# Kernel optimization log

Hardware: AMD Instinct MI355X
Metric: run time of the kernel (lower is better)

## Reference

```python
import jax, jax.numpy as jnp
import numpy as np

POI, EMB, UNITS, QDIM, B = 5000, 256, 512, 256, 64


def setup_inputs() -> dict:
    key = jax.random.key(0)
    ks = jax.random.split(key, 16)
    s = 0.05
    return {
        "x": jax.random.randint(ks[0], (B,), 0, POI),
        "query": jax.random.normal(ks[1], (B, QDIM), jnp.float32),
        "poi_embedding": jax.random.normal(ks[2], (POI, EMB), jnp.float32),
        "A_hat": jax.random.normal(ks[3], (B, B), jnp.float32),
        "dec_hidden": jax.random.normal(ks[4], (B, UNITS), jnp.float32),
        "cat_dec_hidden": jax.random.normal(ks[5], (1, B, UNITS), jnp.float32),
        # GRUCell params (keras order z, r, h; reset_after=True -> bias [2, 3*units])
        "gru_kernel": jax.random.normal(ks[6], (EMB + QDIM, 3 * UNITS), jnp.float32) * s,
        "gru_rec_kernel": jax.random.normal(ks[7], (UNITS, 3 * UNITS), jnp.float32) * s,
        "gru_bias": jax.random.normal(ks[8], (2, 3 * UNITS), jnp.float32) * s,
        # Bahdanau attention params
        "W1_w": jax.random.normal(ks[9], (EMB, UNITS), jnp.float32) * s,
        "W1_b": jnp.zeros((UNITS,), jnp.float32),
        "W2_w": jax.random.normal(ks[10], (UNITS, UNITS), jnp.float32) * s,
        "W2_b": jnp.zeros((UNITS,), jnp.float32),
        "V_w": jax.random.normal(ks[11], (UNITS, 1), jnp.float32) * s,
        "V_b": jnp.zeros((1,), jnp.float32),
        # output dense: concat(context EMB, output_ UNITS, cat_hidden UNITS) -> POI
        "fc_w": jax.random.normal(ks[12], (EMB + 2 * UNITS, POI), jnp.float32) * s,
        "fc_b": jnp.zeros((POI,), jnp.float32),
    }


def _gru_cell(x, h, kernel, rec_kernel, bias):
    # keras GRUCell, reset_after=True, gate order (z, r, h)
    xm = x @ kernel + bias[0]        # [B, 3U]
    hm = h @ rec_kernel + bias[1]    # [B, 3U]
    xz, xr, xh = jnp.split(xm, 3, axis=-1)
    hz, hr, hh = jnp.split(hm, 3, axis=-1)
    z = jax.nn.sigmoid(xz + hz)
    r = jax.nn.sigmoid(xr + hr)
    h_cand = jnp.tanh(xh + r * hh)
    h_new = z * h + (1.0 - z) * h_cand
    return h_new, h_new


def reference(x, query, poi_embedding, A_hat, dec_hidden, cat_dec_hidden,
              gru_kernel, gru_rec_kernel, gru_bias,
              W1_w, W1_b, W2_w, W2_b, V_w, V_b, fc_w, fc_b):
    emb = poi_embedding
    x1 = jnp.concatenate([emb[x], query], axis=1)          # [B, EMB+QDIM]
    output_, state = _gru_cell(x1, dec_hidden, gru_kernel, gru_rec_kernel, gru_bias)
    # Bahdanau attention: values are the full embedding table [POI, EMB]
    v_proj = emb @ W1_w + W1_b                              # [POI, U]
    q_proj = output_ @ W2_w + W2_b                          # [B, U]
    score = jnp.tanh(v_proj[None, :, :] + q_proj[:, None, :]) @ V_w + V_b  # [B, POI, 1]
    attn = jax.nn.softmax(score, axis=1)                    # [B, POI, 1]
    context = jnp.sum(attn * emb[None, :, :], axis=1)       # [B, EMB]
    out_cat = jnp.concatenate([context, output_, cat_dec_hidden[0]], axis=1)
    logits = out_cat @ fc_w + fc_b                          # [B, POI]
    return (logits, state, output_)
```

## Files before the change

### kernel.cpp

```cpp
#include <hip/hip_runtime.h>
#include <hip/hip_bf16.h>

typedef __bf16 bf16;
typedef __bf16 bf16x8 __attribute__((ext_vector_type(8)));
typedef float f32x4 __attribute__((ext_vector_type(4)));

#define BB 64
#define EMB 256
#define UNITS 512
#define POI 5000
#define KCAT 1280
#define SCLD 5024
#define L2E 1.4426950408889634f

__device__ __forceinline__ float rcp_(float x){ return __builtin_amdgcn_rcpf(x); }
__device__ __forceinline__ float exp2_(float x){ return __builtin_amdgcn_exp2f(x); }

__device__ __forceinline__ bf16x8 cvt8(f32x4 a0, f32x4 a1){
  bf16x8 o;
#pragma unroll
  for(int j=0;j<4;j++){ o[j]=(bf16)a0[j]; o[4+j]=(bf16)a1[j]; }
  return o;
}

__device__ __forceinline__ f32x4 mm16r(const float* __restrict__ ap, const float* __restrict__ B,
                                       int ldb, int K, int nc, int lane){
  int q = lane >> 4;
  f32x4 acc = {0.f,0.f,0.f,0.f};
  ap += q*8;
  const float* bp = B + (size_t)(q*8)*ldb + nc;
#pragma unroll 2
  for(int k0 = 0; k0 < K; k0 += 32){
    bf16x8 a = cvt8(*(const f32x4*)ap, *(const f32x4*)(ap+4));
    bf16x8 b;
#pragma unroll
    for(int j=0;j<8;j++) b[j] = (bf16)bp[(size_t)j*ldb];
    acc = __builtin_amdgcn_mfma_f32_16x16x32_bf16(a, b, acc, 0, 0, 0);
    ap += 32; bp += (size_t)32*ldb;
  }
  return acc;
}
__device__ __forceinline__ f32x4 mm16f(const float* __restrict__ A, const float* __restrict__ B,
                                       int lda, int ldb, int K, int mr, int nc, int lane){
  return mm16r(A + (size_t)mr*lda, B, ldb, K, nc, lane);
}

__device__ __forceinline__ void t64(const float* __restrict__ src, int srcLd, int nRv,
    int r0, int c0, int cW, bf16* __restrict__ dstT, int dstLd,
    int lane, int w){
  int r = r0 + lane;
  bool rv = r < nRv;
  int cw4 = cW >> 2;
  int cb = c0 + w*cw4;
  for(int c8=0;c8<cw4;c8+=8){
    int c = cb + c8;
    f32x4 v0={0.f,0.f,0.f,0.f}, v1={0.f,0.f,0.f,0.f};
    if(rv){ v0 = *(const f32x4*)(src + (size_t)r*srcLd + c);
            v1 = *(const f32x4*)(src + (size_t)r*srcLd + c + 4); }
#pragma unroll
    for(int j=0;j<4;j++){
      dstT[(size_t)(c+j)*dstLd + r]   = (bf16)v0[j];
      dstT[(size_t)(c+4+j)*dstLd + r] = (bf16)v1[j];
    }
  }
}

__global__ __launch_bounds__(256) void k_prep0(
    const float* __restrict__ emb, const float* __restrict__ W1, const float* __restrict__ W2,
    const float* __restrict__ fcb, const float* __restrict__ catd,
    float* __restrict__ out, float* __restrict__ outc,
    bf16* __restrict__ embB, bf16* __restrict__ W1Tb, bf16* __restrict__ W2Tb,
    float* __restrict__ sumb, float* __restrict__ sc){
  int bx = blockIdx.x, t = threadIdx.x, lane = t & 63, w = t >> 6;
  if(bx < 80){
    int r0 = bx*64;
    for(int ch = t; ch < 2048; ch += 256){
      int r = r0 + (ch >> 5), cc = (ch & 31)*8;
      if(r < POI){
        f32x4 v0 = *(const f32x4*)(emb + (size_t)r*EMB + cc);
        f32x4 v1 = *(const f32x4*)(emb + (size_t)r*EMB + cc + 4);
        *(bf16x8*)(embB + (size_t)r*EMB + cc) = cvt8(v0, v1);
      }
    }
  } else if(bx < 88){
    int i = bx - 80;
    t64(W1, UNITS, EMB, (i>>1)*64, (i&1)*256, 256, W1Tb, EMB, lane, w);
  } else if(bx < 104){
    int i = bx - 88;
    t64(W2, UNITS, UNITS, (i>>1)*64, (i&1)*256, 256, W2Tb, UNITS, lane, w);
  } else if(bx < 168){
    int b = bx - 104;
    for(int n=t; n<POI; n+=256) out[(size_t)b*POI + n] = fcb[n];
  } else if(bx < 176){
    int base = (bx - 168)*8;
    for(int i=t; i<8*768; i+=256){
      int bb = base + i/768, c = i - (i/768)*768;
      if(c < 256) outc[(size_t)bb*KCAT + c] = 0.f;
      else        outc[(size_t)bb*KCAT + 512 + c] = catd[(size_t)bb*512 + (c-256)];
    }
  } else {
    if(t < BB) sumb[t] = 0.f;
    for(int i=t; i<BB*24; i+=256){
      int b = i/24, j = i - (i/24)*24;
      sc[(size_t)b*SCLD + POI + j] = 0.f;
    }
  }
}

__global__ __launch_bounds__(256) void k_gru(const int* __restrict__ x, const float* __restrict__ query,
    const bf16* __restrict__ embB, const float* __restrict__ h0,
    const float* __restrict__ gruK, const float* __restrict__ gruR,
    float* __restrict__ xmP, float* __restrict__ hmP){
  int lane = threadIdx.x & 63, w = threadIdx.x >> 6;
  int col = blockIdx.x*16 + (lane & 15);
  int y = blockIdx.y, z = blockIdx.z;
  int mr = w*16 + (lane & 15);
  int q = lane >> 4;
  const float* bp = (y ? gruR : gruK) + (size_t)(z*256 + q*8)*1536 + col;
  float* C = (y ? hmP : xmP) + (size_t)z*BB*1536;
  f32x4 acc = {0.f,0.f,0.f,0.f};
  if(y == 0 && z == 0){
    const bf16* ap = embB + (size_t)x[mr]*EMB + q*8;
#pragma unroll 2
    for(int k0=0;k0<256;k0+=32){
      bf16x8 a = *(const bf16x8*)ap;
      bf16x8 b;
#pragma unroll
      for(int j=0;j<8;j++) b[j] = (bf16)bp[(size_t)j*1536];
      acc = __builtin_amdgcn_mfma_f32_16x16x32_bf16(a, b, acc, 0,0,0);
      ap += 32; bp += (size_t)32*1536;
    }
  } else {
    const float* apf = y ? (h0 + (size_t)mr*512 + z*256 + q*8)
                         : (query + (size_t)mr*256 + q*8);
#pragma unroll 2
    for(int k0=0;k0<256;k0+=32){
      bf16x8 a = cvt8(*(const f32x4*)apf, *(const f32x4*)(apf+4));
      bf16x8 b;
#pragma unroll
      for(int j=0;j<8;j++) b[j] = (bf16)bp[(size_t)j*1536];
      acc = __builtin_amdgcn_mfma_f32_16x16x32_bf16(a, b, acc, 0,0,0);
      apf += 32; bp += (size_t)32*1536;
    }
  }
  int rb = w*16 + (lane >> 4)*4;
#pragma unroll
  for(int r=0;r<4;r++) C[(size_t)(rb+r)*1536 + col] = acc[r];
}

__global__ __launch_bounds__(256) void k_gates(const float* __restrict__ xmP, const float* __restrict__ hmP,
                        const float* __restrict__ bias, const float* __restrict__ h0,
                        float* __restrict__ hn, float* __restrict__ outc, float* __restrict__ dout){
  int b = blockIdx.x, u = blockIdx.y*256 + threadIdx.x;
  const float* x0 = xmP + b*1536; const float* x1s = xmP + (size_t)BB*1536 + b*1536;
  const float* h0s = hmP + b*1536; const float* h1s = hmP + (size_t)BB*1536 + b*1536;
  float xz = x0[u]      + x1s[u]      + bias[u];
  float xg = x0[512+u]  + x1s[512+u]  + bias[512+u];
  float xh = x0[1024+u] + x1s[1024+u] + bias[1024+u];
  float hz = h0s[u]      + h1s[u]      + bias[1536+u];
  float hg = h0s[512+u]  + h1s[512+u]  + bias[2048+u];
  float hh = h0s[1024+u] + h1s[1024+u] + bias[2560+u];
  float z = rcp_(1.f + exp2_(-L2E*(xz+hz)));
  float r = rcp_(1.f + exp2_(-L2E*(xg+hg)));
  float ca = xh + r*hh;
  ca = fminf(fmaxf(ca, -15.f), 15.f);
  float e = exp2_(2.f*L2E*ca);
  float hc = (e - 1.f)*rcp_(e + 1.f);
  float h = h0[(size_t)b*512+u];
  float v = z*h + (1.f - z)*hc;
  hn[(size_t)b*512+u] = v;
  outc[(size_t)b*KCAT + 256 + u] = v;
  dout[(size_t)POI*BB + (size_t)b*512 + u] = v;
  dout[(size_t)POI*BB + (size_t)BB*512 + (size_t)b*512 + u] = v;
}

__global__ __launch_bounds__(256) void k_qproj(const float* __restrict__ hn, const bf16* __restrict__ W2Tb,
                        const float* __restrict__ W2b, float* __restrict__ Eq){
  __shared__ float accs[16][17];
  int t = threadIdx.x, lane = t & 63, w = t >> 6;
  int c16 = blockIdx.x & 31, r16 = blockIdx.x >> 5;
  for(int i=t;i<16*17;i+=256) ((float*)accs)[i] = 0.f;
  __syncthreads();
  int q = lane >> 4;
  int mr  = r16*16 + (lane & 15);
  int col = c16*16 + (lane & 15);
  const float* ap = hn + (size_t)mr*UNITS + w*128 + q*8;
  const bf16*  bp = W2Tb + (size_t)col*UNITS + w*128 + q*8;
  f32x4 acc = {0.f,0.f,0.f,0.f};
#pragma unroll
  for(int k0=0;k0<128;k0+=32){
    bf16x8 a = cvt8(*(const f32x4*)ap, *(const f32x4*)(ap+4));
    bf16x8 b = *(const bf16x8*)bp;
    acc = __builtin_amdgcn_mfma_f32_16x16x32_bf16(a,b,acc,0,0,0);
    ap += 32; bp += 32;
  }
#pragma unroll
  for(int r=0;r<4;r++) atomicAdd(&accs[q*4+r][lane & 15], acc[r]);
  __syncthreads();
  int r = t >> 4, c = t & 15;
  int colg = c16*16 + c;
  float v = (accs[r][c] + W2b[colg])*(2.f*L2E);
  Eq[(size_t)(r16*16+r)*UNITS + colg] = exp2_(fminf(fmaxf(v,-40.f),40.f));
}

__global__ __launch_bounds__(256, 8) void k_vscore(
    const bf16* __restrict__ embB, const bf16* __restrict__ W1Tb,
    const float* __restrict__ W1b, const float* __restrict__ Eq,
    const float* __restrict__ Vw, float* __restrict__ scS){
  __shared__ float evsT[64][20];
  __shared__ float vws[64];
  int t = threadIdx.x, lane = t & 63, w = t >> 6;
  int p0 = blockIdx.x*16, uh = blockIdx.y*64;
  int q = lane >> 4;
  int mr = p0 + (lane & 15); if(mr > POI-1) mr = POI-1;
  {
    int colL = w*16 + (lane & 15);
    const bf16* ap = embB + (size_t)mr*EMB + q*8;
    const bf16* bp = W1Tb + (size_t)(uh+colL)*EMB + q*8;
    f32x4 acc = {0.f,0.f,0.f,0.f};
#pragma unroll
    for(int k0=0;k0<EMB;k0+=32){
      bf16x8 a = *(const bf16x8*)ap, b = *(const bf16x8*)bp;
      acc = __builtin_amdgcn_mfma_f32_16x16x32_bf16(a,b,acc,0,0,0);
      ap += 32; bp += 32;
    }
    float bn = W1b[uh+colL];
    f32x4 ev;
#pragma unroll
    for(int r=0;r<4;r++){
      float v = (acc[r] + bn)*(2.f*L2E);
      ev[r] = exp2_(fminf(fmaxf(v,-40.f),40.f));
    }
    *(f32x4*)&evsT[colL][q*4] = ev;
  }
  if(t < 64) vws[t] = Vw[uh + t];
  __syncthreads();
  int pg = t & 3, b = t >> 2;
  const float* qrow = Eq + (size_t)b*UNITS + uh;
  f32x4 s = {0.f,0.f,0.f,0.f};
#pragma unroll 4
  for(int u4=0; u4<16; ++u4){
    f32x4 q4 = *(const f32x4*)&qrow[u4*4];
    f32x4 wv = *(const f32x4*)&vws[u4*4];
#pragma unroll
    for(int j=0;j<4;j++){
      f32x4 ev = *(const f32x4*)&evsT[u4*4+j][4*pg];
#pragma unroll
      for(int e=0;e<4;e++)
        s[e] += wv[j]*rcp_(ev[e]*q4[j] + 1.f);
    }
  }
  int pA = p0 + 4*pg;
  float* srow = scS + (size_t)blockIdx.y*BB*SCLD + (size_t)b*SCLD + pA;
  if(pA + 3 < POI) *(f32x4*)srow = s;
  else {
#pragma unroll
    for(int e=0;e<4;e++) if(pA+e < POI) srow[e] = s[e];
  }
}

__global__ __launch_bounds__(256) void k_smax(float* __restrict__ sc, float* __restrict__ sumb){
  __shared__ float red[256];
  int b = blockIdx.x, y = blockIdx.y, t = threadIdx.x;
  float* sA = sc + (size_t)b*SCLD;
  int pend = (y+1)*640; if(pend > POI) pend = POI;
  float sm = 0.f;
  for(int p = y*640 + t; p < pend; p += 256){
    float acc = sA[p];
#pragma unroll
    for(int s2=1;s2<8;s2++) acc += sA[(size_t)s2*BB*SCLD + p];
    float e = exp2_(-2.f*L2E*acc);
    sA[p] = e;
    sm += e;
  }
  red[t] = sm; __syncthreads();
  for(int o=128;o>0;o>>=1){ if(t<o) red[t]+=red[t+o]; __syncthreads(); }
  if(t==0) atomicAdd(sumb + b, red[0]);
}

__global__ __launch_bounds__(256) void k_ctx(const float* __restrict__ wb, const float* __restrict__ emb,
                                             const float* __restrict__ sumb, float* __restrict__ outc){
  int lane = threadIdx.x & 63, w = threadIdx.x >> 6;
  int n = blockIdx.x*16 + (lane & 15);
  int ky = blockIdx.y;
  int kbeg = ky*64;
  int mr = w*16 + (lane & 15);
  int q = lane >> 4;
  const float* ap = wb + (size_t)mr*SCLD + kbeg + q*8;
  f32x4 acc = {0.f,0.f,0.f,0.f};
  if(ky < 78){
    const float* bp = emb + (size_t)(kbeg + q*8)*EMB + n;
#pragma unroll 2
    for(int k0=0;k0<64;k0+=32){
      bf16x8 a = cvt8(*(const f32x4*)ap, *(const f32x4*)(ap+4));
      bf16x8 b;
#pragma unroll
      for(int j=0;j<8;j++) b[j] = (bf16)bp[(size_t)j*EMB];
      acc = __builtin_amdgcn_mfma_f32_16x16x32_bf16(a,b,acc,0,0,0);
      ap += 32; bp += (size_t)32*EMB;
    }
  } else {
    bf16x8 a = cvt8(*(const f32x4*)ap, *(const f32x4*)(ap+4));
    bf16x8 b;
#pragma unroll
    for(int j=0;j<8;j++){
      int k = kbeg + q*8 + j; int kc = k < POI ? k : POI-1;
      b[j] = (bf16)emb[(size_t)kc*EMB + n];
    }
    acc = __builtin_amdgcn_mfma_f32_16x16x32_bf16(a,b,acc,0,0,0);
  }
  int rb = w*16 + (lane >> 4)*4;
#pragma unroll
  for(int r=0;r<4;r++) atomicAdd(&outc[(size_t)(rb+r)*KCAT + n], acc[r]*rcp_(sumb[rb+r]));
}

__global__ __launch_bounds__(256) void k_logits(const float* __restrict__ A, const float* __restrict__ Bw,
                        float* __restrict__ out){
  int lane = threadIdx.x & 63, w = threadIdx.x >> 6;
  int n = blockIdx.x*16 + (lane & 15);
  int nc = n < POI ? n : POI-1;
  int ky = blockIdx.y, kbeg = ky*320;
  f32x4 acc = mm16f(A + kbeg, Bw + (size_t)kbeg*POI, KCAT, POI, 320,
                    w*16 + (lane & 15), nc, lane);
  int rb = w*16 + (lane >> 4)*4;
  if(n < POI){
#pragma unroll
    for(int r=0;r<4;r++) atomicAdd(&out[(size_t)(rb+r)*POI + n], acc[r]);
  }
}

extern "C" void kernel_launch(void* const* d_in, const int* in_sizes, int n_in,
                              void* d_out, int out_size, void* d_ws, size_t ws_size,
                              hipStream_t stream){
  const int*   x     = (const int*)d_in[0];
  const float* query = (const float*)d_in[1];
  const float* emb   = (const float*)d_in[2];
  const float* h0    = (const float*)d_in[4];
  const float* catd  = (const float*)d_in[5];
  const float* gruK  = (const float*)d_in[6];
  const float* gruR  = (const float*)d_in[7];
  const float* gruB  = (const float*)d_in[8];
  const float* W1    = (const float*)d_in[9];
  const float* W1b   = (const float*)d_in[10];
  const float* W2    = (const float*)d_in[11];
  const float* W2b   = (const float*)d_in[12];
  const float* Vw    = (const float*)d_in[13];
  const float* fcw   = (const float*)d_in[15];
  const float* fcb   = (const float*)d_in[16];
  float* out = (float*)d_out;

  char* ws = (char*)d_ws;
  size_t off = 0;
  auto alloc = [&](size_t bytes)->void*{ void* p = ws + off; off += (bytes + 255) & ~(size_t)255; return p; };
  float* outc   = (float*)alloc((size_t)BB*KCAT*4);
  float* xmP    = (float*)alloc((size_t)2*BB*1536*4);
  float* hmP    = (float*)alloc((size_t)2*BB*1536*4);
  float* hn     = (float*)alloc((size_t)BB*512*4);
  float* Eq     = (float*)alloc((size_t)BB*512*4);
  bf16*  embB   = (bf16*)alloc((size_t)POI*EMB*2);
  bf16*  W1Tb   = (bf16*)alloc((size_t)UNITS*EMB*2);
  bf16*  W2Tb   = (bf16*)alloc((size_t)UNITS*UNITS*2);
  float* sumb   = (float*)alloc((size_t)BB*4);
  float* sc     = (float*)alloc((size_t)8*BB*SCLD*4);

  k_prep0  <<<177, 256, 0, stream>>>(emb, W1, W2, fcb, catd, out, outc,
                                     embB, W1Tb, W2Tb, sumb, sc);
  k_gru    <<<dim3(96,2,2), 256, 0, stream>>>(x, query, embB, h0, gruK, gruR, xmP, hmP);
  k_gates  <<<dim3(BB,2), 256, 0, stream>>>(xmP, hmP, gruB, h0, hn, outc, out);
  k_qproj  <<<128, 256, 0, stream>>>(hn, W2Tb, W2b, Eq);
  k_vscore <<<dim3(313,8), 256, 0, stream>>>(embB, W1Tb, W1b, Eq, Vw, sc);
  k_smax   <<<dim3(BB,8), 256, 0, stream>>>(sc, sumb);
  k_ctx    <<<dim3(16,79), 256, 0, stream>>>(sc, emb, sumb, outc);
  k_logits <<<dim3(313,4), 256, 0, stream>>>(outc, fcw, out);
}
```

Baseline: 191.2 us.

## Pre-transpose weights to K-major bf16 for vectorized MFMA B-operand loads

```diff
diff --git a/kernel.cpp b/kernel.cpp
--- a/kernel.cpp
+++ b/kernel.cpp
@@ -23,30 +23,8 @@
   return o;
 }
 
-__device__ __forceinline__ f32x4 mm16r(const float* __restrict__ ap, const float* __restrict__ B,
-                                       int ldb, int K, int nc, int lane){
-  int q = lane >> 4;
-  f32x4 acc = {0.f,0.f,0.f,0.f};
-  ap += q*8;
-  const float* bp = B + (size_t)(q*8)*ldb + nc;
-#pragma unroll 2
-  for(int k0 = 0; k0 < K; k0 += 32){
-    bf16x8 a = cvt8(*(const f32x4*)ap, *(const f32x4*)(ap+4));
-    bf16x8 b;
-#pragma unroll
-    for(int j=0;j<8;j++) b[j] = (bf16)bp[(size_t)j*ldb];
-    acc = __builtin_amdgcn_mfma_f32_16x16x32_bf16(a, b, acc, 0, 0, 0);
-    ap += 32; bp += (size_t)32*ldb;
-  }
-  return acc;
-}
-__device__ __forceinline__ f32x4 mm16f(const float* __restrict__ A, const float* __restrict__ B,
-                                       int lda, int ldb, int K, int mr, int nc, int lane){
-  return mm16r(A + (size_t)mr*lda, B, ldb, K, nc, lane);
-}
-
 __device__ __forceinline__ void t64(const float* __restrict__ src, int srcLd, int nRv,
-    int r0, int c0, int cW, bf16* __restrict__ dstT, int dstLd,
+    int r0, int c0, int cW, bf16* __restrict__ dstT, int dstLd, int dstRmax,
     int lane, int w){
   int r = r0 + lane;
   bool rv = r < nRv;
@@ -57,19 +35,24 @@
     f32x4 v0={0.f,0.f,0.f,0.f}, v1={0.f,0.f,0.f,0.f};
     if(rv){ v0 = *(const f32x4*)(src + (size_t)r*srcLd + c);
             v1 = *(const f32x4*)(src + (size_t)r*srcLd + c + 4); }
-#pragma unroll
-    for(int j=0;j<4;j++){
-      dstT[(size_t)(c+j)*dstLd + r]   = (bf16)v0[j];
-      dstT[(size_t)(c+4+j)*dstLd + r] = (bf16)v1[j];
+    if(r < dstRmax){
+#pragma unroll
+      for(int j=0;j<4;j++){
+        dstT[(size_t)(c+j)*dstLd + r]   = (bf16)v0[j];
+        dstT[(size_t)(c+4+j)*dstLd + r] = (bf16)v1[j];
+      }
     }
   }
 }
 
 __global__ __launch_bounds__(256) void k_prep0(
     const float* __restrict__ emb, const float* __restrict__ W1, const float* __restrict__ W2,
+    const float* __restrict__ gruK, const float* __restrict__ gruR, const float* __restrict__ fcw,
     const float* __restrict__ fcb, const float* __restrict__ catd,
     float* __restrict__ out, float* __restrict__ outc,
     bf16* __restrict__ embB, bf16* __restrict__ W1Tb, bf16* __restrict__ W2Tb,
+    bf16* __restrict__ embTb, bf16* __restrict__ gruKTb, bf16* __restrict__ gruRTb,
+    bf16* __restrict__ fcwT,
     float* __restrict__ sumb, float* __restrict__ sc){
   int bx = blockIdx.x, t = threadIdx.x, lane = t & 63, w = t >> 6;
   if(bx < 80){
@@ -84,10 +67,10 @@
     }
   } else if(bx < 88){
     int i = bx - 80;
-    t64(W1, UNITS, EMB, (i>>1)*64, (i&1)*256, 256, W1Tb, EMB, lane, w);
+    t64(W1, UNITS, EMB, (i>>1)*64, (i&1)*256, 256, W1Tb, EMB, EMB, lane, w);
   } else if(bx < 104){
     int i = bx - 88;
-    t64(W2, UNITS, UNITS, (i>>1)*64, (i&1)*256, 256, W2Tb, UNITS, lane, w);
+    t64(W2, UNITS, UNITS, (i>>1)*64, (i&1)*256, 256, W2Tb, UNITS, UNITS, lane, w);
   } else if(bx < 168){
     int b = bx - 104;
     for(int n=t; n<POI; n+=256) out[(size_t)b*POI + n] = fcb[n];
@@ -98,49 +81,68 @@
       if(c < 256) outc[(size_t)bb*KCAT + c] = 0.f;
       else        outc[(size_t)bb*KCAT + 512 + c] = catd[(size_t)bb*512 + (c-256)];
     }
-  } else {
+  } else if(bx == 176){
     if(t < BB) sumb[t] = 0.f;
     for(int i=t; i<BB*24; i+=256){
       int b = i/24, j = i - (i/24)*24;
       sc[(size_t)b*SCLD + POI + j] = 0.f;
     }
+  } else if(bx < 337){
+    int i = bx - 177;
+    t64(emb, EMB, POI, (i>>1)*64, (i&1)*128, 128, embTb, SCLD, SCLD, lane, w);
+  } else if(bx < 401){
+    int i = bx - 337;
+    t64(gruK, 1536, 512, (i>>3)*64, (i&7)*192, 192, gruKTb, 512, 512, lane, w);
+  } else if(bx < 465){
+    int i = bx - 401;
+    t64(gruR, 1536, 512, (i>>3)*64, (i&7)*192, 192, gruRTb, 512, 512, lane, w);
+  } else {
+    int i = bx - 465;
+    int kt = i/40, nt = i - kt*40;
+    int k = kt*64 + lane;
+    int cb = nt*128 + w*32;
+    for(int cc=0; cc<32; cc+=8){
+      int c = cb + cc;
+      if(c < POI){
+        f32x4 v0 = *(const f32x4*)(fcw + (size_t)k*POI + c);
+        f32x4 v1 = *(const f32x4*)(fcw + (size_t)k*POI + c + 4);
+#pragma unroll
+        for(int j=0;j<4;j++){
+          fcwT[(size_t)(c+j)*KCAT + k]   = (bf16)v0[j];
+          fcwT[(size_t)(c+4+j)*KCAT + k] = (bf16)v1[j];
+        }
+      }
+    }
   }
 }
 
 __global__ __launch_bounds__(256) void k_gru(const int* __restrict__ x, const float* __restrict__ query,
     const bf16* __restrict__ embB, const float* __restrict__ h0,
-    const float* __restrict__ gruK, const float* __restrict__ gruR,
+    const bf16* __restrict__ gruKTb, const bf16* __restrict__ gruRTb,
     float* __restrict__ xmP, float* __restrict__ hmP){
   int lane = threadIdx.x & 63, w = threadIdx.x >> 6;
   int col = blockIdx.x*16 + (lane & 15);
   int y = blockIdx.y, z = blockIdx.z;
   int mr = w*16 + (lane & 15);
   int q = lane >> 4;
-  const float* bp = (y ? gruR : gruK) + (size_t)(z*256 + q*8)*1536 + col;
+  const bf16* bp = (y ? gruRTb : gruKTb) + (size_t)col*512 + z*256 + q*8;
   float* C = (y ? hmP : xmP) + (size_t)z*BB*1536;
   f32x4 acc = {0.f,0.f,0.f,0.f};
   if(y == 0 && z == 0){
     const bf16* ap = embB + (size_t)x[mr]*EMB + q*8;
-#pragma unroll 2
+#pragma unroll
     for(int k0=0;k0<256;k0+=32){
-      bf16x8 a = *(const bf16x8*)ap;
-      bf16x8 b;
-#pragma unroll
-      for(int j=0;j<8;j++) b[j] = (bf16)bp[(size_t)j*1536];
-      acc = __builtin_amdgcn_mfma_f32_16x16x32_bf16(a, b, acc, 0,0,0);
-      ap += 32; bp += (size_t)32*1536;
+      acc = __builtin_amdgcn_mfma_f32_16x16x32_bf16(*(const bf16x8*)ap, *(const bf16x8*)bp, acc, 0,0,0);
+      ap += 32; bp += 32;
     }
   } else {
     const float* apf = y ? (h0 + (size_t)mr*512 + z*256 + q*8)
                          : (query + (size_t)mr*256 + q*8);
-#pragma unroll 2
+#pragma unroll
     for(int k0=0;k0<256;k0+=32){
       bf16x8 a = cvt8(*(const f32x4*)apf, *(const f32x4*)(apf+4));
-      bf16x8 b;
-#pragma unroll
-      for(int j=0;j<8;j++) b[j] = (bf16)bp[(size_t)j*1536];
-      acc = __builtin_amdgcn_mfma_f32_16x16x32_bf16(a, b, acc, 0,0,0);
-      apf += 32; bp += (size_t)32*1536;
+      acc = __builtin_amdgcn_mfma_f32_16x16x32_bf16(a, *(const bf16x8*)bp, acc, 0,0,0);
+      apf += 32; bp += 32;
     }
   }
   int rb = w*16 + (lane >> 4)*4;
@@ -278,50 +280,46 @@
   if(t==0) atomicAdd(sumb + b, red[0]);
 }
 
-__global__ __launch_bounds__(256) void k_ctx(const float* __restrict__ wb, const float* __restrict__ emb,
+__global__ __launch_bounds__(256) void k_ctx(const float* __restrict__ wb, const bf16* __restrict__ embTb,
                                              const float* __restrict__ sumb, float* __restrict__ outc){
   int lane = threadIdx.x & 63, w = threadIdx.x >> 6;
   int n = blockIdx.x*16 + (lane & 15);
   int ky = blockIdx.y;
   int kbeg = ky*64;
+  int K = (ky == 78) ? 32 : 64;
   int mr = w*16 + (lane & 15);
   int q = lane >> 4;
   const float* ap = wb + (size_t)mr*SCLD + kbeg + q*8;
+  const bf16*  bp = embTb + (size_t)n*SCLD + kbeg + q*8;
   f32x4 acc = {0.f,0.f,0.f,0.f};
-  if(ky < 78){
-    const float* bp = emb + (size_t)(kbeg + q*8)*EMB + n;
-#pragma unroll 2
-    for(int k0=0;k0<64;k0+=32){
-      bf16x8 a = cvt8(*(const f32x4*)ap, *(const f32x4*)(ap+4));
-      bf16x8 b;
-#pragma unroll
-      for(int j=0;j<8;j++) b[j] = (bf16)bp[(size_t)j*EMB];
-      acc = __builtin_amdgcn_mfma_f32_16x16x32_bf16(a,b,acc,0,0,0);
-      ap += 32; bp += (size_t)32*EMB;
-    }
-  } else {
+  for(int k0=0;k0<K;k0+=32){
     bf16x8 a = cvt8(*(const f32x4*)ap, *(const f32x4*)(ap+4));
-    bf16x8 b;
-#pragma unroll
-    for(int j=0;j<8;j++){
-      int k = kbeg + q*8 + j; int kc = k < POI ? k : POI-1;
-      b[j] = (bf16)emb[(size_t)kc*EMB + n];
-    }
+    bf16x8 b = *(const bf16x8*)bp;
     acc = __builtin_amdgcn_mfma_f32_16x16x32_bf16(a,b,acc,0,0,0);
+    ap += 32; bp += 32;
   }
   int rb = w*16 + (lane >> 4)*4;
 #pragma unroll
   for(int r=0;r<4;r++) atomicAdd(&outc[(size_t)(rb+r)*KCAT + n], acc[r]*rcp_(sumb[rb+r]));
 }
 
-__global__ __launch_bounds__(256) void k_logits(const float* __restrict__ A, const float* __restrict__ Bw,
+__global__ __launch_bounds__(256) void k_logits(const float* __restrict__ A, const bf16* __restrict__ BT,
                         float* __restrict__ out){
   int lane = threadIdx.x & 63, w = threadIdx.x >> 6;
   int n = blockIdx.x*16 + (lane & 15);
   int nc = n < POI ? n : POI-1;
   int ky = blockIdx.y, kbeg = ky*320;
-  f32x4 acc = mm16f(A + kbeg, Bw + (size_t)kbeg*POI, KCAT, POI, 320,
-                    w*16 + (lane & 15), nc, lane);
+  int q = lane >> 4;
+  const float* ap = A + (size_t)(w*16 + (lane & 15))*KCAT + kbeg + q*8;
+  const bf16*  bp = BT + (size_t)nc*KCAT + kbeg + q*8;
+  f32x4 acc = {0.f,0.f,0.f,0.f};
+#pragma unroll 2
+  for(int k0=0;k0<320;k0+=32){
+    bf16x8 a = cvt8(*(const f32x4*)ap, *(const f32x4*)(ap+4));
+    bf16x8 b = *(const bf16x8*)bp;
+    acc = __builtin_amdgcn_mfma_f32_16x16x32_bf16(a,b,acc,0,0,0);
+    ap += 32; bp += 32;
+  }
   int rb = w*16 + (lane >> 4)*4;
   if(n < POI){
 #pragma unroll
@@ -360,16 +358,20 @@
   bf16*  embB   = (bf16*)alloc((size_t)POI*EMB*2);
   bf16*  W1Tb   = (bf16*)alloc((size_t)UNITS*EMB*2);
   bf16*  W2Tb   = (bf16*)alloc((size_t)UNITS*UNITS*2);
+  bf16*  embTb  = (bf16*)alloc((size_t)EMB*SCLD*2);
+  bf16*  gruKTb = (bf16*)alloc((size_t)1536*512*2);
+  bf16*  gruRTb = (bf16*)alloc((size_t)1536*512*2);
+  bf16*  fcwT   = (bf16*)alloc((size_t)POI*KCAT*2);
   float* sumb   = (float*)alloc((size_t)BB*4);
   float* sc     = (float*)alloc((size_t)8*BB*SCLD*4);
 
-  k_prep0  <<<177, 256, 0, stream>>>(emb, W1, W2, fcb, catd, out, outc,
-                                     embB, W1Tb, W2Tb, sumb, sc);
-  k_gru    <<<dim3(96,2,2), 256, 0, stream>>>(x, query, embB, h0, gruK, gruR, xmP, hmP);
+  k_prep0  <<<1265, 256, 0, stream>>>(emb, W1, W2, gruK, gruR, fcw, fcb, catd, out, outc,
+                                      embB, W1Tb, W2Tb, embTb, gruKTb, gruRTb, fcwT, sumb, sc);
+  k_gru    <<<dim3(96,2,2), 256, 0, stream>>>(x, query, embB, h0, gruKTb, gruRTb, xmP, hmP);
   k_gates  <<<dim3(BB,2), 256, 0, stream>>>(xmP, hmP, gruB, h0, hn, outc, out);
   k_qproj  <<<128, 256, 0, stream>>>(hn, W2Tb, W2b, Eq);
   k_vscore <<<dim3(313,8), 256, 0, stream>>>(embB, W1Tb, W1b, Eq, Vw, sc);
   k_smax   <<<dim3(BB,8), 256, 0, stream>>>(sc, sumb);
-  k_ctx    <<<dim3(16,79), 256, 0, stream>>>(sc, emb, sumb, outc);
-  k_logits <<<dim3(313,4), 256, 0, stream>>>(outc, fcw, out);
-}
+  k_ctx    <<<dim3(16,79), 256, 0, stream>>>(sc, embTb, sumb, outc);
+  k_logits <<<dim3(313,4), 256, 0, stream>>>(outc, fcwT, out);
+}
```

Result: slower. 201.0 us (+5.1%).
